# Kernel tuning notes

Hardware: AMD Instinct MI355X
Metric: run time of the kernel (lower is better)

## Reference

```python
import jax, jax.numpy as jnp
import numpy as np

B, T, C, H = 4, 2048, 1024, 16
HD = C // H  # head dim = 64

def setup_inputs() -> dict:
    key = jax.random.key(0)
    k1, k2, k3 = jax.random.split(key, 3)
    x = jax.random.normal(k1, (B, T, C), dtype=jnp.float32)
    w_attn = jax.random.normal(k2, (C, 3 * C), dtype=jnp.float32) * 0.02
    w_proj = jax.random.normal(k3, (C, C), dtype=jnp.float32) * 0.02
    return {"x": x, "w_attn": w_attn, "w_proj": w_proj}

def reference(x, w_attn, w_proj):
    b, t, c = x.shape
    qkv = x @ w_attn  # [B,T,3C]
    q, k, v = jnp.split(qkv, 3, axis=-1)
    # [B,T,C] -> [B,H,T,HD]
    def heads(z):
        return z.reshape(b, t, H, HD).transpose(0, 2, 1, 3)
    q, k, v = heads(q), heads(k), heads(v)
    scale = 1.0 / jnp.sqrt(jnp.float32(HD))
    att = jnp.einsum('bhqd,bhkd->bhqk', q, k) * scale  # [B,H,T,T]
    causal = jnp.tril(jnp.ones((t, t), dtype=bool))
    att = jnp.where(causal[None, None], att, -jnp.inf)
    att = jax.nn.softmax(att, axis=-1)
    y = jnp.einsum('bhqk,bhkd->bhqd', att, v)  # [B,H,T,HD]
    y = y.transpose(0, 2, 1, 3).reshape(b, t, c)
    return y @ w_proj
```

## Files before the change

kernel.cpp:

```cpp
#include <hip/hip_runtime.h>
#include <hip/hip_bf16.h>

typedef short bf16x8 __attribute__((ext_vector_type(8)));
typedef short short4v __attribute__((ext_vector_type(4)));
typedef float f32x4 __attribute__((ext_vector_type(4)));
typedef float f32x16 __attribute__((ext_vector_type(16)));

template <bool V> struct BoolC { static constexpr bool value = V; };

__device__ __forceinline__ short f2b(float f) {
  __hip_bfloat16 h = __float2bfloat16(f);
  union { __hip_bfloat16 h; short s; } u; u.h = h; return u.s;
}

__device__ __forceinline__ unsigned cvtpk_bf16(float lo, float hi) {
  unsigned r;
  asm("v_cvt_pk_bf16_f32 %0, %1, %2" : "=v"(r) : "v"(lo), "v"(hi));
  return r;
}

__device__ __forceinline__ f32x16 mfma32(bf16x8 a, bf16x8 b, f32x16 c) {
  return __builtin_amdgcn_mfma_f32_32x32x16_bf16(a, b, c, 0, 0, 0);
}

__device__ __forceinline__ void async_copy16(const short* g, short* l) {
  __builtin_amdgcn_global_load_lds((const __attribute__((address_space(1))) void*)g,
                                   (__attribute__((address_space(3))) void*)l, 16, 0, 0);
}

__global__ __launch_bounds__(256) void pre_kernel(const float* __restrict__ x, short* __restrict__ xb,
                                                  const float* __restrict__ wa, short* __restrict__ waT,
                                                  const float* __restrict__ wp, short* __restrict__ wpT,
                                                  float qscale) {
  const int tid = threadIdx.x;
  const int blk = blockIdx.x;
  if (blk < 8192) {
    const int i = blk * 256 + tid;
    const float4 v = ((const float4*)x)[i];
    short4v o;
    o[0] = f2b(v.x); o[1] = f2b(v.y); o[2] = f2b(v.z); o[3] = f2b(v.w);
    ((short4v*)xb)[i] = o;
    return;
  }
  __shared__ float t[32][33];
  const float* in; short* out;
  int idx, gxb, Cn, qrows; float qs;
  if (blk < 11264) { idx = blk - 8192;  in = wa; out = waT; gxb = 96; Cn = 3072; qrows = 1024; qs = qscale; }
  else             { idx = blk - 11264; in = wp; out = wpT; gxb = 32; Cn = 1024; qrows = 0;    qs = 1.0f; }
  const int bx = idx % gxb, by = idx / gxb;
  const int tx = tid & 31, ty = tid >> 5;
  const int c0 = bx * 32, r0 = by * 32;
#pragma unroll
  for (int yy = 0; yy < 32; yy += 8)
    t[ty + yy][tx] = in[(size_t)(r0 + ty + yy) * Cn + (c0 + tx)];
  __syncthreads();
#pragma unroll
  for (int yy = 0; yy < 32; yy += 8) {
    const int orow = c0 + ty + yy;
    float v = t[tx][ty + yy];
    if (orow < qrows) v *= qs;
    out[(size_t)orow * 1024 + (r0 + tx)] = f2b(v);
  }
}

__global__ __launch_bounds__(256) void vtrans_kernel(const short* __restrict__ qkv,
                                                     short* __restrict__ vT) {
  constexpr int T = 2048, C3 = 3072, HD = 64;
  const int bh = blockIdx.y, b = bh >> 4, h = bh & 15;
  const int t0 = blockIdx.x * 64;
  __shared__ short tile[64][72];
  const int tid = threadIdx.x;
  const int tr = tid >> 2, dc = (tid & 3) * 16;
  const short* src = qkv + (size_t)b * T * C3 + (size_t)(t0 + tr) * C3 + 2048 + h * HD + dc;
  *(bf16x8*)&tile[tr][dc] = *(const bf16x8*)src;
  *(bf16x8*)&tile[tr][dc + 8] = *(const bf16x8*)(src + 8);
  __syncthreads();
  const int dr = tid >> 2, tc = (tid & 3) * 16;
  bf16x8 o0, o1;
#pragma unroll
  for (int i = 0; i < 8; i++) o0[i] = tile[tc + i][dr];
#pragma unroll
  for (int i = 0; i < 8; i++) o1[i] = tile[tc + 8 + i][dr];
  short* dst = vT + ((size_t)bh * HD + dr) * T + t0 + tc;
  *(bf16x8*)dst = o0;
  *(bf16x8*)(dst + 8) = o1;
}

template <int BN, typename OutT>
__global__ __launch_bounds__(512, 2) void gemm8p_kernel(const short* __restrict__ A,
                                                        const short* __restrict__ Bt,
                                                        OutT* __restrict__ C,
                                                        int M, int N, int K) {
  constexpr int NB = BN / 64;
  constexpr int NSTREAM = NB + 4;
  __shared__ short ldsA[2][16384];
  __shared__ short ldsB[2][NB * 4096];

  const int tid = threadIdx.x;
  const int w = tid >> 6, lane = tid & 63;
  const int quad = lane >> 4, l16 = lane & 15;
  const int half = w >> 2;
  const int wn = (w & 3) * (BN / 4);
  const int wm = half * 128;

  const int gx = gridDim.x;
  const int nwg = gx * gridDim.y;
  const int flat = blockIdx.y * gx + blockIdx.x;
  const int swz = (flat & 7) * (nwg >> 3) + (flat >> 3);
  const int bn = swz % gx, bm = swz / gx;
  const int m0 = bm * 256, n0 = bn * BN;

  const int rsub = lane >> 3;
  const int cl = (lane & 7) ^ rsub;
  const short* pAsrc = A + (size_t)(m0 + half * 128 + (w & 3) * 8 + rsub) * K + cl * 8;
  const short* pBsrc = Bt + (size_t)(n0 + w * 8 + rsub) * K + cl * 8;
  const int dstoff = w * 512;

  f32x4 acc[8][NB] = {};
  bf16x8 bfr[NB][2];

  auto issue = [&](int i, int buf, int tt) {
    if (i < NB)
      async_copy16(pBsrc + (size_t)(i * 64) * K + tt * 64, &ldsB[buf][i * 4096 + dstoff]);
    else
      async_copy16(pAsrc + (size_t)((i - NB) * 32) * K + tt * 64,
                   &ldsA[buf][(i - NB) * 4096 + dstoff]);
  };

#pragma unroll
  for (int i = 0; i < NSTREAM; ++i) issue(i, 0, 0);

  const int NT = K >> 6;

#define GEMM_PHASE(P, GS, GL)                                                                  \
  {                                                                                            \
    if constexpr (LAST) { asm volatile("s_waitcnt vmcnt(" #GL ")" ::: "memory"); }             \
    else                { asm volatile("s_waitcnt vmcnt(" #GS ")" ::: "memory"); }             \
    __builtin_amdgcn_s_barrier();                                                              \
    asm volatile("" ::: "memory");                                                             \
    bf16x8 af[2][2];                                                                           \
    _Pragma("unroll") for (int mm = 0; mm < 2; ++mm)                                           \
    _Pragma("unroll") for (int kh = 0; kh < 2; ++kh)                                           \
      af[mm][kh] = *(const bf16x8*)&ldsA[buf][((P * 2 + half) * 32 + mm * 16 + l16) * 64 +     \
                                              (((kh * 4 + quad) ^ (l16 & 7)) * 8)];            \
    if constexpr (P == 0) {                                                                    \
      _Pragma("unroll") for (int nf = 0; nf < NB; ++nf)                                        \
      _Pragma("unroll") for (int kh = 0; kh < 2; ++kh)                                         \
        bfr[nf][kh] = *(const bf16x8*)&ldsB[buf][(wn + nf * 16 + l16) * 64 +                   \
                                                 (((kh * 4 + quad) ^ (l16 & 7)) * 8)];         \
    }                                                                                          \
    if constexpr (!LAST) {                                                                     \
      if constexpr (2 * P < NSTREAM) issue(2 * P, buf ^ 1, t + 1);                             \
      if constexpr (2 * P + 1 < NSTREAM) issue(2 * P + 1, buf ^ 1, t + 1);                     \
    }                                                                                          \
    __builtin_amdgcn_s_setprio(1);                                                             \
    _Pragma("unroll") for (int mm = 0; mm < 2; ++mm)                                           \
    _Pragma("unroll") for (int nf = 0; nf < NB; ++nf) {                                        \
      acc[P * 2 + mm][nf] = __builtin_amdgcn_mfma_f32_16x16x32_bf16(af[mm][0], bfr[nf][0],     \
                                                                    acc[P * 2 + mm][nf], 0, 0, 0); \
      acc[P * 2 + mm][nf] = __builtin_amdgcn_mfma_f32_16x16x32_bf16(af[mm][1], bfr[nf][1],     \
                                                                    acc[P * 2 + mm][nf], 0, 0, 0); \
    }                                                                                          \
    __builtin_amdgcn_s_setprio(0);                                                             \
    __builtin_amdgcn_s_barrier();                                                              \
  }

  auto tile = [&](int t, auto lastc) {
    constexpr bool LAST = decltype(lastc)::value;
    const int buf = t & 1;
    GEMM_PHASE(0, 3, 3)
    GEMM_PHASE(1, 4, 2)
    GEMM_PHASE(2, 5, 1)
    GEMM_PHASE(3, 6, 0)
  };

  for (int t = 0; t < NT - 1; ++t) tile(t, BoolC<false>{});
  tile(NT - 1, BoolC<true>{});
#undef GEMM_PHASE

  (void)M;
#pragma unroll
  for (int mf = 0; mf < 8; ++mf)
#pragma unroll
    for (int nf = 0; nf < NB; ++nf) {
      const int col = n0 + wn + nf * 16 + l16;
#pragma unroll
      for (int r = 0; r < 4; ++r) {
        const int row = m0 + wm + mf * 16 + quad * 4 + r;
        if constexpr (sizeof(OutT) == 4)
          C[(size_t)row * N + col] = acc[mf][nf][r];
        else
          C[(size_t)row * N + col] = f2b(acc[mf][nf][r]);
      }
    }
}

__global__ __launch_bounds__(256, 2) void attn_kernel(const short* __restrict__ qkv,
                                                      const short* __restrict__ vT,
                                                      short* __restrict__ y) {
  constexpr int T = 2048, C3 = 3072, Cc = 1024, HD = 64;
  const int f = blockIdx.y * 8 + blockIdx.x;
  const int bh = (f & 7) * 8 + ((f >> 3) & 7);
  const int xb = f >> 6;
  const int b = bh >> 4, h = bh & 15;
  const int tid = threadIdx.x, lane = tid & 63, wave = tid >> 6;
  const int l32 = lane & 31, hi = lane >> 5;

  __shared__ short Ksb[2][64 * 64];
  __shared__ short Vtb[2][64 * 64];

  const size_t base = (size_t)b * T * C3;
  const int qcol = h * HD, kcol = Cc + h * HD;
  const size_t vtbase = (size_t)bh * HD * T;

  const int r8 = lane >> 3;
  const int cg8 = ((lane & 7) ^ r8) * 8;
  const short* gk[2];
  const short* gv[2];
  short* lk[2][2]; short* lv[2][2];
#pragma unroll
  for (int t8 = 0; t8 < 2; t8++) {
    const int row = wave * 16 + t8 * 8 + r8;
    gk[t8] = qkv + base + (size_t)row * C3 + kcol + cg8;
    gv[t8] = vT + vtbase + (size_t)row * T + cg8;
#pragma unroll
    for (int bu = 0; bu < 2; bu++) {
      lk[bu][t8] = &Ksb[bu][(wave * 16 + t8 * 8) * 64];
      lv[bu][t8] = &Vtb[bu][(wave * 16 + t8 * 8) * 64];
    }
  }
  const int rs7 = l32 & 7;

  bf16x8 ones;
#pragma unroll
  for (int i = 0; i < 8; i++) ones[i] = (short)0x3F80;

  for (int half = 0; half < 2; half++) {
    const int t = half ? xb : (15 - xb);
    const int q0 = t * 128;
    const int jmax = 2 * t + 1;
    const int jd = 2 * t + (wave >> 1);
    const int qrow = q0 + wave * 32 + l32;

    bf16x8 qf[4];
    {
      const short* qp = qkv + base + (size_t)qrow * C3 + qcol + hi * 8;
#pragma unroll
      for (int wk = 0; wk < 4; wk++) qf[wk] = *(const bf16x8*)(qp + wk * 16);
    }

    f32x16 o0 = {}, o1 = {}, lC = {};

    async_copy16(gk[0], lk[0][0]);
    async_copy16(gk[1], lk[0][1]);
    async_copy16(gv[0], lv[0][0]);
    async_copy16(gv[1], lv[0][1]);

    for (int j = 0; j <= jmax; j++) {
      const int cur = j & 1;
      __syncthreads();

      if (j < jmax) {
        const size_t ko = (size_t)(j + 1) * 64 * C3;
        const int vo = (j + 1) * 64;
        async_copy16(gk[0] + ko, lk[cur ^ 1][0]);
        async_copy16(gk[1] + ko, lk[cur ^ 1][1]);
        async_copy16(gv[0] + vo, lv[cur ^ 1][0]);
        async_copy16(gv[1] + vo, lv[cur ^ 1][1]);
      }

      if (j > jd) continue;

      const bool up = (64 * j + 32) <= (q0 + wave * 32 + 31);

      f32x16 st0 = {}, st1 = {};
      __builtin_amdgcn_s_setprio(1);
#pragma unroll
      for (int wk = 0; wk < 4; wk++) {
        const bf16x8 k0 = *(const bf16x8*)&Ksb[cur][l32 * 64 + (((2 * wk + hi) ^ rs7) * 8)];
        st0 = mfma32(k0, qf[wk], st0);
      }
      if (up) {
#pragma unroll
        for (int wk = 0; wk < 4; wk++) {
          const bf16x8 k1 = *(const bf16x8*)&Ksb[cur][(32 + l32) * 64 + (((2 * wk + hi) ^ rs7) * 8)];
          st1 = mfma32(k1, qf[wk], st1);
        }
      }
      __builtin_amdgcn_s_setprio(0);

      if (j == jd) {
#pragma unroll
        for (int r = 0; r < 16; r++) {
          const int kvl = 64 * j + (r & 3) + 8 * (r >> 2) + 4 * hi;
          if (kvl > qrow) st0[r] = -INFINITY;
          if (up && (kvl + 32 > qrow)) st1[r] = -INFINITY;
        }
      }

      bf16x8 vf00, vf01, vf10, vf11, vf02, vf03, vf12, vf13;
      vf00 = *(const bf16x8*)&Vtb[cur][l32 * 64 + (((0 + hi) ^ rs7) * 8)];
      vf01 = *(const bf16x8*)&Vtb[cur][l32 * 64 + (((2 + hi) ^ rs7) * 8)];
      vf10 = *(const bf16x8*)&Vtb[cur][(32 + l32) * 64 + (((0 + hi) ^ rs7) * 8)];
      vf11 = *(const bf16x8*)&Vtb[cur][(32 + l32) * 64 + (((2 + hi) ^ rs7) * 8)];
      if (up) {
        vf02 = *(const bf16x8*)&Vtb[cur][l32 * 64 + (((4 + hi) ^ rs7) * 8)];
        vf03 = *(const bf16x8*)&Vtb[cur][l32 * 64 + (((6 + hi) ^ rs7) * 8)];
        vf12 = *(const bf16x8*)&Vtb[cur][(32 + l32) * 64 + (((4 + hi) ^ rs7) * 8)];
        vf13 = *(const bf16x8*)&Vtb[cur][(32 + l32) * 64 + (((6 + hi) ^ rs7) * 8)];
      }

#pragma unroll
      for (int r = 0; r < 16; r++) st0[r] = __builtin_amdgcn_exp2f(st0[r]);
      bf16x8 pa0, pa1, pa2, pa3;
      {
        unsigned a0 = cvtpk_bf16(st0[0], st0[1]), c0 = cvtpk_bf16(st0[2], st0[3]);
        unsigned b0 = cvtpk_bf16(st0[4], st0[5]), d0 = cvtpk_bf16(st0[6], st0[7]);
        asm volatile("v_permlane32_swap_b32 %0, %1" : "+v"(a0), "+v"(b0));
        asm volatile("v_permlane32_swap_b32 %0, %1" : "+v"(c0), "+v"(d0));
        union { unsigned u[4]; bf16x8 v; } p; p.u[0] = a0; p.u[1] = c0; p.u[2] = b0; p.u[3] = d0;
        pa0 = p.v;
        unsigned a1 = cvtpk_bf16(st0[8], st0[9]), c1 = cvtpk_bf16(st0[10], st0[11]);
        unsigned b1 = cvtpk_bf16(st0[12], st0[13]), d1 = cvtpk_bf16(st0[14], st0[15]);
        asm volatile("v_permlane32_swap_b32 %0, %1" : "+v"(a1), "+v"(b1));
        asm volatile("v_permlane32_swap_b32 %0, %1" : "+v"(c1), "+v"(d1));
        union { unsigned u[4]; bf16x8 v; } q; q.u[0] = a1; q.u[1] = c1; q.u[2] = b1; q.u[3] = d1;
        pa1 = q.v;
      }
      if (up) {
#pragma unroll
        for (int r = 0; r < 16; r++) st1[r] = __builtin_amdgcn_exp2f(st1[r]);
        unsigned a2 = cvtpk_bf16(st1[0], st1[1]), c2 = cvtpk_bf16(st1[2], st1[3]);
        unsigned b2 = cvtpk_bf16(st1[4], st1[5]), d2 = cvtpk_bf16(st1[6], st1[7]);
        asm volatile("v_permlane32_swap_b32 %0, %1" : "+v"(a2), "+v"(b2));
        asm volatile("v_permlane32_swap_b32 %0, %1" : "+v"(c2), "+v"(d2));
        union { unsigned u[4]; bf16x8 v; } p; p.u[0] = a2; p.u[1] = c2; p.u[2] = b2; p.u[3] = d2;
        pa2 = p.v;
        unsigned a3 = cvtpk_bf16(st1[8], st1[9]), c3 = cvtpk_bf16(st1[10], st1[11]);
        unsigned b3 = cvtpk_bf16(st1[12], st1[13]), d3 = cvtpk_bf16(st1[14], st1[15]);
        asm volatile("v_permlane32_swap_b32 %0, %1" : "+v"(a3), "+v"(b3));
        asm volatile("v_permlane32_swap_b32 %0, %1" : "+v"(c3), "+v"(d3));
        union { unsigned u[4]; bf16x8 v; } q; q.u[0] = a3; q.u[1] = c3; q.u[2] = b3; q.u[3] = d3;
        pa3 = q.v;
      }

      __builtin_amdgcn_s_setprio(1);
      lC = mfma32(pa0, ones, lC);
      lC = mfma32(pa1, ones, lC);
      o0 = mfma32(pa0, vf00, o0);
      o0 = mfma32(pa1, vf01, o0);
      o1 = mfma32(pa0, vf10, o1);
      o1 = mfma32(pa1, vf11, o1);
      if (up) {
        lC = mfma32(pa2, ones, lC);
        lC = mfma32(pa3, ones, lC);
        o0 = mfma32(pa2, vf02, o0);
        o0 = mfma32(pa3, vf03, o0);
        o1 = mfma32(pa2, vf12, o1);
        o1 = mfma32(pa3, vf13, o1);
      }
      __builtin_amdgcn_s_setprio(0);
    }

#pragma unroll
    for (int r = 0; r < 16; r++) {
      const int rq = (r & 3) + 8 * (r >> 2) + 4 * hi;
      const int row_g = q0 + wave * 32 + rq;
      const float inv = 1.0f / lC[r];
      short* yp = y + (size_t)(b * T + row_g) * Cc + h * HD;
      yp[l32] = f2b(o0[r] * inv);
      yp[32 + l32] = f2b(o1[r] * inv);
    }
  }
}

extern "C" void kernel_launch(void* const* d_in, const int* in_sizes, int n_in,
                              void* d_out, int out_size, void* d_ws, size_t ws_size,
                              hipStream_t stream) {
  constexpr int B = 4, T = 2048, C = 1024;
  constexpr int M = B * T;
  constexpr int N1 = 3 * C;
  const float* x      = (const float*)d_in[0];
  const float* w_attn = (const float*)d_in[1];
  const float* w_proj = (const float*)d_in[2];
  float* out = (float*)d_out;

  char* ws = (char*)d_ws;
  short* xb   = (short*)(ws + 0);
  short* waT  = (short*)(ws + 16777216);
  short* wpT  = (short*)(ws + 23068672);
  short* qkvb = (short*)(ws + 25165824);
  short* yb   = (short*)(ws + 75497472);
  short* vT   = xb;

  const float qscale = 0.125f * 1.44269504088896340736f;

  pre_kernel<<<12288, 256, 0, stream>>>(x, xb, w_attn, waT, w_proj, wpT, qscale);
  gemm8p_kernel<192, short><<<dim3(N1 / 192, M / 256), 512, 0, stream>>>(xb, waT, qkvb, M, N1, C);
  vtrans_kernel<<<dim3(T / 64, B * 16), 256, 0, stream>>>(qkvb, vT);
  attn_kernel<<<dim3(8, B * 16), 256, 0, stream>>>(qkvb, vT, yb);
  gemm8p_kernel<128, float><<<dim3(C / 128, M / 256), 512, 0, stream>>>(yb, wpT, out, M, C, C);
}
```

Baseline: 229.2 us.

## Software-pipeline LDS fragment reads one phase ahead in bf16 GEMM mainloop

Restructures the GEMM main loop so that A and B fragments for the next phase are read from LDS into double-buffered registers before the current phase's MFMAs run. This overlaps LDS read latency with matrix math and removes one barrier per phase. B fragments for the next K-tile are prefetched in the last phase, and the loop is unrolled by two to alternate register buffers. It costs more VGPRs, which could lower occupancy or cause spills, and it retunes the vmcnt waits by hand, which is fragile.

Measured after the change: 224.0 us. -2.3%, faster.

```diff
diff --git a/kernel.cpp b/kernel.cpp
--- a/kernel.cpp
+++ b/kernel.cpp
@@ -21,6 +21,15 @@
 
 __device__ __forceinline__ f32x16 mfma32(bf16x8 a, bf16x8 b, f32x16 c) {
   return __builtin_amdgcn_mfma_f32_32x32x16_bf16(a, b, c, 0, 0, 0);
+}
+
+template <int N> __device__ __forceinline__ void vmwait() {
+  if constexpr (N == 0) asm volatile("s_waitcnt vmcnt(0)" ::: "memory");
+  else if constexpr (N == 1) asm volatile("s_waitcnt vmcnt(1)" ::: "memory");
+  else if constexpr (N == 2) asm volatile("s_waitcnt vmcnt(2)" ::: "memory");
+  else if constexpr (N == 3) asm volatile("s_waitcnt vmcnt(3)" ::: "memory");
+  else if constexpr (N == 4) asm volatile("s_waitcnt vmcnt(4)" ::: "memory");
+  else asm volatile("s_waitcnt vmcnt(5)" ::: "memory");
 }
 
 __device__ __forceinline__ void async_copy16(const short* g, short* l) {
@@ -117,7 +126,8 @@
   const int dstoff = w * 512;
 
   f32x4 acc[8][NB] = {};
-  bf16x8 bfr[NB][2];
+  bf16x8 bfA[NB][2], bfB[NB][2];
+  bf16x8 afA[2][2], afB[2][2];
 
   auto issue = [&](int i, int buf, int tt) {
     if (i < NB)
@@ -126,57 +136,79 @@
       async_copy16(pAsrc + (size_t)((i - NB) * 32) * K + tt * 64,
                    &ldsA[buf][(i - NB) * 4096 + dstoff]);
   };
+  auto readA = [&](bf16x8 (&dst)[2][2], int buf, int chunk) {
+#pragma unroll
+    for (int mm = 0; mm < 2; ++mm)
+#pragma unroll
+      for (int kh = 0; kh < 2; ++kh)
+        dst[mm][kh] = *(const bf16x8*)&ldsA[buf][((chunk * 2 + half) * 32 + mm * 16 + l16) * 64 +
+                                                 (((kh * 4 + quad) ^ (l16 & 7)) * 8)];
+  };
+  auto readB = [&](bf16x8 (&dst)[NB][2], int buf) {
+#pragma unroll
+    for (int nf = 0; nf < NB; ++nf)
+#pragma unroll
+      for (int kh = 0; kh < 2; ++kh)
+        dst[nf][kh] = *(const bf16x8*)&ldsB[buf][(wn + nf * 16 + l16) * 64 +
+                                                 (((kh * 4 + quad) ^ (l16 & 7)) * 8)];
+  };
+
+#define MFMA_CL(P, AF, BF)                                                                     \
+  __builtin_amdgcn_s_setprio(1);                                                               \
+  _Pragma("unroll") for (int mm = 0; mm < 2; ++mm)                                             \
+  _Pragma("unroll") for (int nf = 0; nf < NB; ++nf) {                                          \
+    acc[(P)*2 + mm][nf] = __builtin_amdgcn_mfma_f32_16x16x32_bf16((AF)[mm][0], (BF)[nf][0],    \
+                                                                  acc[(P)*2 + mm][nf], 0, 0, 0); \
+    acc[(P)*2 + mm][nf] = __builtin_amdgcn_mfma_f32_16x16x32_bf16((AF)[mm][1], (BF)[nf][1],    \
+                                                                  acc[(P)*2 + mm][nf], 0, 0, 0); \
+  }                                                                                            \
+  __builtin_amdgcn_s_setprio(0);
 
 #pragma unroll
   for (int i = 0; i < NSTREAM; ++i) issue(i, 0, 0);
+  vmwait<3>();
+  __builtin_amdgcn_s_barrier();
+  readB(bfA, 0);
+  readA(afA, 0, 0);
+
+  auto tileb = [&](int buf, auto lastc, int tnext, auto& bfc, auto& bfn) {
+    constexpr bool LASTT = decltype(lastc)::value;
+    constexpr int g1 = LASTT ? 1 : 3;
+    constexpr int g2 = LASTT ? 0 : 4;
+    constexpr int g3 = LASTT ? 0 : (NB == 3 ? 2 : 3);
+    vmwait<2>();
+    __builtin_amdgcn_s_barrier();
+    readA(afB, buf, 1);
+    if constexpr (!LASTT) { issue(0, buf ^ 1, tnext); issue(1, buf ^ 1, tnext); }
+    MFMA_CL(0, afA, bfc)
+    vmwait<g1>();
+    __builtin_amdgcn_s_barrier();
+    readA(afA, buf, 2);
+    if constexpr (!LASTT) { issue(2, buf ^ 1, tnext); issue(3, buf ^ 1, tnext); }
+    MFMA_CL(1, afB, bfc)
+    vmwait<g2>();
+    __builtin_amdgcn_s_barrier();
+    readA(afB, buf, 3);
+    if constexpr (!LASTT) { issue(4, buf ^ 1, tnext); issue(5, buf ^ 1, tnext); }
+    MFMA_CL(2, afA, bfc)
+    vmwait<g3>();
+    __builtin_amdgcn_s_barrier();
+    if constexpr (!LASTT) {
+      readB(bfn, buf ^ 1);
+      readA(afA, buf ^ 1, 0);
+      if constexpr (6 < NSTREAM) issue(6, buf ^ 1, tnext);
+    }
+    MFMA_CL(3, afB, bfc)
+  };
 
   const int NT = K >> 6;
-
-#define GEMM_PHASE(P, GS, GL)                                                                  \
-  {                                                                                            \
-    if constexpr (LAST) { asm volatile("s_waitcnt vmcnt(" #GL ")" ::: "memory"); }             \
-    else                { asm volatile("s_waitcnt vmcnt(" #GS ")" ::: "memory"); }             \
-    __builtin_amdgcn_s_barrier();                                                              \
-    asm volatile("" ::: "memory");                                                             \
-    bf16x8 af[2][2];                                                                           \
-    _Pragma("unroll") for (int mm = 0; mm < 2; ++mm)                                           \
-    _Pragma("unroll") for (int kh = 0; kh < 2; ++kh)                                           \
-      af[mm][kh] = *(const bf16x8*)&ldsA[buf][((P * 2 + half) * 32 + mm * 16 + l16) * 64 +     \
-                                              (((kh * 4 + quad) ^ (l16 & 7)) * 8)];            \
-    if constexpr (P == 0) {                                                                    \
-      _Pragma("unroll") for (int nf = 0; nf < NB; ++nf)                                        \
-      _Pragma("unroll") for (int kh = 0; kh < 2; ++kh)                                         \
-        bfr[nf][kh] = *(const bf16x8*)&ldsB[buf][(wn + nf * 16 + l16) * 64 +                   \
-                                                 (((kh * 4 + quad) ^ (l16 & 7)) * 8)];         \
-    }                                                                                          \
-    if constexpr (!LAST) {                                                                     \
-      if constexpr (2 * P < NSTREAM) issue(2 * P, buf ^ 1, t + 1);                             \
-      if constexpr (2 * P + 1 < NSTREAM) issue(2 * P + 1, buf ^ 1, t + 1);                     \
-    }                                                                                          \
-    __builtin_amdgcn_s_setprio(1);                                                             \
-    _Pragma("unroll") for (int mm = 0; mm < 2; ++mm)                                           \
-    _Pragma("unroll") for (int nf = 0; nf < NB; ++nf) {                                        \
-      acc[P * 2 + mm][nf] = __builtin_amdgcn_mfma_f32_16x16x32_bf16(af[mm][0], bfr[nf][0],     \
-                                                                    acc[P * 2 + mm][nf], 0, 0, 0); \
-      acc[P * 2 + mm][nf] = __builtin_amdgcn_mfma_f32_16x16x32_bf16(af[mm][1], bfr[nf][1],     \
-                                                                    acc[P * 2 + mm][nf], 0, 0, 0); \
-    }                                                                                          \
-    __builtin_amdgcn_s_setprio(0);                                                             \
-    __builtin_amdgcn_s_barrier();                                                              \
+  for (int t = 0; t < NT - 2; t += 2) {
+    tileb(0, BoolC<false>{}, t + 1, bfA, bfB);
+    tileb(1, BoolC<false>{}, t + 2, bfB, bfA);
   }
-
-  auto tile = [&](int t, auto lastc) {
-    constexpr bool LAST = decltype(lastc)::value;
-    const int buf = t & 1;
-    GEMM_PHASE(0, 3, 3)
-    GEMM_PHASE(1, 4, 2)
-    GEMM_PHASE(2, 5, 1)
-    GEMM_PHASE(3, 6, 0)
-  };
-
-  for (int t = 0; t < NT - 1; ++t) tile(t, BoolC<false>{});
-  tile(NT - 1, BoolC<true>{});
-#undef GEMM_PHASE
+  tileb(0, BoolC<false>{}, NT - 1, bfA, bfB);
+  tileb(1, BoolC<true>{}, 0, bfB, bfA);
+#undef MFMA_CL
 
   (void)M;
 #pragma unroll
```

## Shrink GEMM tiles to 128-row blocks with 4 waves and fewer barriers

Applied to the files above, without the earlier changes.

Both GEMMs switch from 512-thread, 256-row workgroups to 256-thread, 128-row workgroups, which doubles the grid and halves LDS per block. The load-issue schedule is regenerated for the new stream count, and the trailing barrier in each phase is dropped, relying on the lgkmcnt/vmcnt waits plus the leading barrier. This aims to improve occupancy and CU fill and to cut barrier overhead, at the cost of less A/B reuse per block and a possible LDS race now that the second barrier is gone.

New measurement: 226.8 us. No clear change (-1.0%).

```diff
diff --git a/kernel.cpp b/kernel.cpp
--- a/kernel.cpp
+++ b/kernel.cpp
@@ -21,6 +21,18 @@
 
 __device__ __forceinline__ f32x16 mfma32(bf16x8 a, bf16x8 b, f32x16 c) {
   return __builtin_amdgcn_mfma_f32_32x32x16_bf16(a, b, c, 0, 0, 0);
+}
+
+template <int N> __device__ __forceinline__ void vmwait() {
+  if constexpr (N == 0) asm volatile("s_waitcnt vmcnt(0)" ::: "memory");
+  else if constexpr (N == 1) asm volatile("s_waitcnt vmcnt(1)" ::: "memory");
+  else if constexpr (N == 2) asm volatile("s_waitcnt vmcnt(2)" ::: "memory");
+  else if constexpr (N == 3) asm volatile("s_waitcnt vmcnt(3)" ::: "memory");
+  else if constexpr (N == 4) asm volatile("s_waitcnt vmcnt(4)" ::: "memory");
+  else if constexpr (N == 5) asm volatile("s_waitcnt vmcnt(5)" ::: "memory");
+  else if constexpr (N == 6) asm volatile("s_waitcnt vmcnt(6)" ::: "memory");
+  else if constexpr (N == 7) asm volatile("s_waitcnt vmcnt(7)" ::: "memory");
+  else asm volatile("s_waitcnt vmcnt(8)" ::: "memory");
 }
 
 __device__ __forceinline__ void async_copy16(const short* g, short* l) {
@@ -87,96 +99,102 @@
 }
 
 template <int BN, typename OutT>
-__global__ __launch_bounds__(512, 2) void gemm8p_kernel(const short* __restrict__ A,
+__global__ __launch_bounds__(256, 2) void gemm2b_kernel(const short* __restrict__ A,
                                                         const short* __restrict__ Bt,
                                                         OutT* __restrict__ C,
                                                         int M, int N, int K) {
   constexpr int NB = BN / 64;
-  constexpr int NSTREAM = NB + 4;
-  __shared__ short ldsA[2][16384];
-  __shared__ short ldsB[2][NB * 4096];
+  constexpr int NBU = BN / 32;
+  constexpr int NSTREAM = NBU + 4;
+  __shared__ short ldsA[2][128 * 64];
+  __shared__ short ldsB[2][BN * 64];
 
   const int tid = threadIdx.x;
   const int w = tid >> 6, lane = tid & 63;
   const int quad = lane >> 4, l16 = lane & 15;
-  const int half = w >> 2;
-  const int wn = (w & 3) * (BN / 4);
-  const int wm = half * 128;
+  const int wn = w * (BN / 4);
 
   const int gx = gridDim.x;
   const int nwg = gx * gridDim.y;
   const int flat = blockIdx.y * gx + blockIdx.x;
   const int swz = (flat & 7) * (nwg >> 3) + (flat >> 3);
   const int bn = swz % gx, bm = swz / gx;
-  const int m0 = bm * 256, n0 = bn * BN;
+  const int m0 = bm * 128, n0 = bn * BN;
 
   const int rsub = lane >> 3;
   const int cl = (lane & 7) ^ rsub;
-  const short* pAsrc = A + (size_t)(m0 + half * 128 + (w & 3) * 8 + rsub) * K + cl * 8;
+  const short* pAsrc = A + (size_t)(m0 + w * 8 + rsub) * K + cl * 8;
   const short* pBsrc = Bt + (size_t)(n0 + w * 8 + rsub) * K + cl * 8;
-  const int dstoff = w * 512;
 
   f32x4 acc[8][NB] = {};
   bf16x8 bfr[NB][2];
 
   auto issue = [&](int i, int buf, int tt) {
-    if (i < NB)
-      async_copy16(pBsrc + (size_t)(i * 64) * K + tt * 64, &ldsB[buf][i * 4096 + dstoff]);
+    if (i < NBU)
+      async_copy16(pBsrc + (size_t)(i * 32) * K + tt * 64, &ldsB[buf][(i * 32 + w * 8) * 64]);
     else
-      async_copy16(pAsrc + (size_t)((i - NB) * 32) * K + tt * 64,
-                   &ldsA[buf][(i - NB) * 4096 + dstoff]);
+      async_copy16(pAsrc + (size_t)((i - NBU) * 32) * K + tt * 64,
+                   &ldsA[buf][((i - NBU) * 32 + w * 8) * 64]);
   };
-
-#pragma unroll
-  for (int i = 0; i < NSTREAM; ++i) issue(i, 0, 0);
-
-  const int NT = K >> 6;
-
-#define GEMM_PHASE(P, GS, GL)                                                                  \
+  auto readA = [&](bf16x8 (&af)[2][2], int buf, int P) {
+#pragma unroll
+    for (int mm = 0; mm < 2; ++mm)
+#pragma unroll
+      for (int kh = 0; kh < 2; ++kh)
+        af[mm][kh] = *(const bf16x8*)&ldsA[buf][(P * 32 + mm * 16 + l16) * 64 +
+                                                (((kh * 4 + quad) ^ (l16 & 7)) * 8)];
+  };
+  auto readB = [&](int buf) {
+#pragma unroll
+    for (int nf = 0; nf < NB; ++nf)
+#pragma unroll
+      for (int kh = 0; kh < 2; ++kh)
+        bfr[nf][kh] = *(const bf16x8*)&ldsB[buf][(wn + nf * 16 + l16) * 64 +
+                                                 (((kh * 4 + quad) ^ (l16 & 7)) * 8)];
+  };
+
+#define PHASE(P)                                                                               \
   {                                                                                            \
-    if constexpr (LAST) { asm volatile("s_waitcnt vmcnt(" #GL ")" ::: "memory"); }             \
-    else                { asm volatile("s_waitcnt vmcnt(" #GS ")" ::: "memory"); }             \
+    constexpr int ISS0 = (NSTREAM + 3) >> 2, ISS1 = (NSTREAM + 2) >> 2,                        \
+                  ISS2 = (NSTREAM + 1) >> 2;                                                   \
+    constexpr int CUM = ((P) > 0 ? ISS0 : 0) + ((P) > 1 ? ISS1 : 0) + ((P) > 2 ? ISS2 : 0);    \
+    constexpr int GS = NSTREAM - (NBU + 1 + (P)) + CUM;                                        \
+    constexpr int GL = 3 - (P);                                                                \
+    if constexpr ((P) == 0) asm volatile("s_waitcnt lgkmcnt(0)" ::: "memory");                 \
+    if constexpr (LAST) vmwait<GL>(); else vmwait<GS>();                                       \
     __builtin_amdgcn_s_barrier();                                                              \
-    asm volatile("" ::: "memory");                                                             \
     bf16x8 af[2][2];                                                                           \
-    _Pragma("unroll") for (int mm = 0; mm < 2; ++mm)                                           \
-    _Pragma("unroll") for (int kh = 0; kh < 2; ++kh)                                           \
-      af[mm][kh] = *(const bf16x8*)&ldsA[buf][((P * 2 + half) * 32 + mm * 16 + l16) * 64 +     \
-                                              (((kh * 4 + quad) ^ (l16 & 7)) * 8)];            \
-    if constexpr (P == 0) {                                                                    \
-      _Pragma("unroll") for (int nf = 0; nf < NB; ++nf)                                        \
-      _Pragma("unroll") for (int kh = 0; kh < 2; ++kh)                                         \
-        bfr[nf][kh] = *(const bf16x8*)&ldsB[buf][(wn + nf * 16 + l16) * 64 +                   \
-                                                 (((kh * 4 + quad) ^ (l16 & 7)) * 8)];         \
-    }                                                                                          \
+    readA(af, buf, (P));                                                                       \
+    if constexpr ((P) == 0) readB(buf);                                                        \
     if constexpr (!LAST) {                                                                     \
-      if constexpr (2 * P < NSTREAM) issue(2 * P, buf ^ 1, t + 1);                             \
-      if constexpr (2 * P + 1 < NSTREAM) issue(2 * P + 1, buf ^ 1, t + 1);                     \
+      constexpr int NI = (NSTREAM + 3 - (P)) >> 2;                                             \
+      _Pragma("unroll") for (int ii = 0; ii < NI; ++ii) issue(CUM + ii, buf ^ 1, t + 1);       \
     }                                                                                          \
     __builtin_amdgcn_s_setprio(1);                                                             \
     _Pragma("unroll") for (int mm = 0; mm < 2; ++mm)                                           \
     _Pragma("unroll") for (int nf = 0; nf < NB; ++nf) {                                        \
-      acc[P * 2 + mm][nf] = __builtin_amdgcn_mfma_f32_16x16x32_bf16(af[mm][0], bfr[nf][0],     \
-                                                                    acc[P * 2 + mm][nf], 0, 0, 0); \
-      acc[P * 2 + mm][nf] = __builtin_amdgcn_mfma_f32_16x16x32_bf16(af[mm][1], bfr[nf][1],     \
-                                                                    acc[P * 2 + mm][nf], 0, 0, 0); \
+      acc[(P)*2 + mm][nf] = __builtin_amdgcn_mfma_f32_16x16x32_bf16(af[mm][0], bfr[nf][0],     \
+                                                                    acc[(P)*2 + mm][nf], 0, 0, 0); \
+      acc[(P)*2 + mm][nf] = __builtin_amdgcn_mfma_f32_16x16x32_bf16(af[mm][1], bfr[nf][1],     \
+                                                                    acc[(P)*2 + mm][nf], 0, 0, 0); \
     }                                                                                          \
     __builtin_amdgcn_s_setprio(0);                                                             \
-    __builtin_amdgcn_s_barrier();                                                              \
   }
 
-  auto tile = [&](int t, auto lastc) {
+#pragma unroll
+  for (int i = 0; i < NSTREAM; ++i) issue(i, 0, 0);
+
+  const int NT = K >> 6;
+  auto tile = [&](int t, int buf, auto lastc) {
     constexpr bool LAST = decltype(lastc)::value;
-    const int buf = t & 1;
-    GEMM_PHASE(0, 3, 3)
-    GEMM_PHASE(1, 4, 2)
-    GEMM_PHASE(2, 5, 1)
-    GEMM_PHASE(3, 6, 0)
+    PHASE(0)
+    PHASE(1)
+    PHASE(2)
+    PHASE(3)
   };
-
-  for (int t = 0; t < NT - 1; ++t) tile(t, BoolC<false>{});
-  tile(NT - 1, BoolC<true>{});
-#undef GEMM_PHASE
+  for (int t = 0; t < NT - 1; ++t) tile(t, t & 1, BoolC<false>{});
+  tile(NT - 1, (NT - 1) & 1, BoolC<true>{});
+#undef PHASE
 
   (void)M;
 #pragma unroll
@@ -186,7 +204,7 @@
       const int col = n0 + wn + nf * 16 + l16;
 #pragma unroll
       for (int r = 0; r < 4; ++r) {
-        const int row = m0 + wm + mf * 16 + quad * 4 + r;
+        const int row = m0 + mf * 16 + quad * 4 + r;
         if constexpr (sizeof(OutT) == 4)
           C[(size_t)row * N + col] = acc[mf][nf][r];
         else
@@ -396,8 +414,8 @@
   const float qscale = 0.125f * 1.44269504088896340736f;
 
   pre_kernel<<<12288, 256, 0, stream>>>(x, xb, w_attn, waT, w_proj, wpT, qscale);
-  gemm8p_kernel<192, short><<<dim3(N1 / 192, M / 256), 512, 0, stream>>>(xb, waT, qkvb, M, N1, C);
+  gemm2b_kernel<192, short><<<dim3(N1 / 192, M / 128), 256, 0, stream>>>(xb, waT, qkvb, M, N1, C);
   vtrans_kernel<<<dim3(T / 64, B * 16), 256, 0, stream>>>(qkvb, vT);
   attn_kernel<<<dim3(8, B * 16), 256, 0, stream>>>(qkvb, vT, yb);
-  gemm8p_kernel<128, float><<<dim3(C / 128, M / 256), 512, 0, stream>>>(yb, wpT, out, M, C, C);
-}
+  gemm2b_kernel<128, float><<<dim3(C / 128, M / 128), 256, 0, stream>>>(yb, wpT, out, M, C, C);
+}
```
